# Optimization experiments

Measured on AMD Instinct MI355X. Metric: run time of the kernel, lower is better.

Reference implementation:

```python
import jax, jax.numpy as jnp
import numpy as np

M, I, J = 524288, 16, 16


def setup_inputs() -> dict:
    key = jax.random.key(0)
    k1, k2, k3, k4 = jax.random.split(key, 4)
    h = jax.random.normal(k1, (2, 1, 1, I, J), dtype=jnp.float32)
    gi = jax.random.normal(k2, (2, M, 1, I), dtype=jnp.float32)
    gj = jax.random.normal(k3, (2, 1, M, J), dtype=jnp.float32)
    theta = jax.random.uniform(k4, (2, M), dtype=jnp.float32) * (2.0 * np.pi)
    return {"h": h, "gi": gi, "gj": gj, "theta": theta}


def reference(h, gi, gj, theta):
    # Theta = diag(cos(theta[0])) + 1j * diag(sin(theta[1])) -- diagonal, so the
    # per-(i,j) bilinear form gj_j @ Theta @ gi_i is an O(M) contraction.
    tre = jnp.cos(theta[0])  # [M]
    tim = jnp.sin(theta[1])  # [M]
    a, b = gj[0, 0], gj[1, 0]            # [M, J] real/imag of gj
    e, f = gi[0, :, 0, :], gi[1, :, 0, :]  # [M, I] real/imag of gi
    # u = Theta_diag * gj (complex elementwise along M)
    u_re = a * tre[:, None] - b * tim[:, None]  # [M, J]
    u_im = a * tim[:, None] + b * tre[:, None]  # [M, J]
    # out[i,j] = sum_m gi[m,i] * theta[m] * gj[m,j] (complex)
    out_re = jnp.einsum('mi,mj->ij', e, u_re) - jnp.einsum('mi,mj->ij', f, u_im)
    out_im = jnp.einsum('mi,mj->ij', e, u_im) + jnp.einsum('mi,mj->ij', f, u_re)
    # htilde = h + reflected path, then squeeze the singleton dims -> [2, I, J]
    return h[:, 0, 0] + jnp.stack([out_re, out_im], axis=0)
```

## Files before the change

### kernel.cpp

```cpp
#include <hip/hip_runtime.h>


constexpr int MDIM    = 524288;
constexpr int THREADS = 256;
constexpr int BLOCKS  = 512;
constexpr int SLOTS   = BLOCKS * THREADS / 16;

__global__ void theta_init(const float* __restrict__ h, float* __restrict__ out) {
    int k = blockIdx.x * blockDim.x + threadIdx.x;
    if (k < 512) out[k] = h[k];
}

__device__ __forceinline__ void theta_step(
    const float4 e4, const float4 f4, const float4 a4, const float4 b4,
    const float c, const float s,
    float (&are)[4][4], float (&aim)[4][4])
{
    const float av[4] = {a4.x, a4.y, a4.z, a4.w};
    const float bv[4] = {b4.x, b4.y, b4.z, b4.w};
    const float ev[4] = {e4.x, e4.y, e4.z, e4.w};
    const float fv[4] = {f4.x, f4.y, f4.z, f4.w};
    float ure[4], uim[4];
#pragma unroll
    for (int j = 0; j < 4; ++j) {
        ure[j] = av[j] * c - bv[j] * s;
        uim[j] = av[j] * s + bv[j] * c;
    }
#pragma unroll
    for (int i = 0; i < 4; ++i) {
#pragma unroll
        for (int j = 0; j < 4; ++j) {
            are[i][j] += ev[i] * ure[j] - fv[i] * uim[j];
            aim[i][j] += ev[i] * uim[j] + fv[i] * ure[j];
        }
    }
}

__global__ __launch_bounds__(THREADS) void theta_main(
    const float* __restrict__ gi, const float* __restrict__ gj,
    const float* __restrict__ theta, float* __restrict__ out)
{
    const int t    = threadIdx.x;
    const int g    = blockIdx.x * THREADS + t;
    const int tile = t & 15;
    const int i0   = (tile >> 2) << 2;
    const int j0   = (tile & 3) << 2;
    const int slot = g >> 4;

    const float* e_base = gi + i0;
    const float* f_base = gi + MDIM * 16 + i0;
    const float* a_base = gj + j0;
    const float* b_base = gj + MDIM * 16 + j0;

    float are[4][4] = {{0.f}};
    float aim[4][4] = {{0.f}};

    for (int m = slot; m < MDIM; m += 2 * SLOTS) {
        const int m2 = m + SLOTS;
        const float4 e0 = *(const float4*)(e_base + m * 16);
        const float4 f0 = *(const float4*)(f_base + m * 16);
        const float4 a0 = *(const float4*)(a_base + m * 16);
        const float4 b0 = *(const float4*)(b_base + m * 16);
        const float t00 = theta[m];
        const float t10 = theta[MDIM + m];
        const float4 e1 = *(const float4*)(e_base + m2 * 16);
        const float4 f1 = *(const float4*)(f_base + m2 * 16);
        const float4 a1 = *(const float4*)(a_base + m2 * 16);
        const float4 b1 = *(const float4*)(b_base + m2 * 16);
        const float t01 = theta[m2];
        const float t11 = theta[MDIM + m2];

        const float c0 = __cosf(t00), s0 = __sinf(t10);
        theta_step(e0, f0, a0, b0, c0, s0, are, aim);
        const float c1 = __cosf(t01), s1 = __sinf(t11);
        theta_step(e1, f1, a1, b1, c1, s1, are, aim);
    }

#pragma unroll
    for (int i = 0; i < 4; ++i) {
#pragma unroll
        for (int j = 0; j < 4; ++j) {
            are[i][j] += __shfl_xor(are[i][j], 16);
            are[i][j] += __shfl_xor(are[i][j], 32);
            aim[i][j] += __shfl_xor(aim[i][j], 16);
            aim[i][j] += __shfl_xor(aim[i][j], 32);
        }
    }

    __shared__ float red[4][16][33];
    const int wave = t >> 6;
    const int lane = t & 63;
    if (lane < 16) {
#pragma unroll
        for (int i = 0; i < 4; ++i) {
#pragma unroll
            for (int j = 0; j < 4; ++j) {
                red[wave][lane][i * 4 + j]      = are[i][j];
                red[wave][lane][16 + i * 4 + j] = aim[i][j];
            }
        }
    }
    __syncthreads();

#pragma unroll
    for (int k = 0; k < 2; ++k) {
        const int idx = t * 2 + k;
        const int tl  = idx >> 5;
        const int v   = idx & 31;
        const float sum = red[0][tl][v] + red[1][tl][v] + red[2][tl][v] + red[3][tl][v];
        const int ii  = ((tl >> 2) << 2) + ((v & 15) >> 2);
        const int jj  = ((tl & 3) << 2) + (v & 3);
        const int off = ((v & 16) ? 256 : 0) + ii * 16 + jj;
        atomicAdd(out + off, sum);
    }
}

extern "C" void kernel_launch(void* const* d_in, const int* in_sizes, int n_in,
                              void* d_out, int out_size, void* d_ws, size_t ws_size,
                              hipStream_t stream) {
    const float* h     = (const float*)d_in[0];
    const float* gi    = (const float*)d_in[1];
    const float* gj    = (const float*)d_in[2];
    const float* theta = (const float*)d_in[3];
    float* out = (float*)d_out;

    theta_init<<<2, 256, 0, stream>>>(h, out);
    theta_main<<<BLOCKS, THREADS, 0, stream>>>(gi, gj, theta, out);
}
```

Measured before the change: 174.8 us.

## Quadruple grid, add occupancy hint, replace atomics with workspace partial reduction

Raises the grid from 512 to 2048 blocks with an 8-waves launch bound to increase memory-level parallelism on the bandwidth-bound contraction. When workspace is available, each block writes its 512 partial sums to a buffer and a separate reduce kernel adds them plus h, avoiding atomics and the init kernel. Risks register spilling from the occupancy bound and an extra launch with strided partial reads; falls back to the atomic path if workspace is too small.

After: 312.2 us. +78.6%, slower.

```diff
diff --git a/kernel.cpp b/kernel.cpp
--- a/kernel.cpp
+++ b/kernel.cpp
@@ -3,13 +3,8 @@
 
 constexpr int MDIM    = 524288;
 constexpr int THREADS = 256;
-constexpr int BLOCKS  = 512;
+constexpr int BLOCKS  = 2048;
 constexpr int SLOTS   = BLOCKS * THREADS / 16;
-
-__global__ void theta_init(const float* __restrict__ h, float* __restrict__ out) {
-    int k = blockIdx.x * blockDim.x + threadIdx.x;
-    if (k < 512) out[k] = h[k];
-}
 
 __device__ __forceinline__ void theta_step(
     const float4 e4, const float4 f4, const float4 a4, const float4 b4,
@@ -36,9 +31,10 @@
     }
 }
 
-__global__ __launch_bounds__(THREADS) void theta_main(
+template <bool USE_ATOMIC>
+__device__ __forceinline__ void theta_body(
     const float* __restrict__ gi, const float* __restrict__ gj,
-    const float* __restrict__ theta, float* __restrict__ out)
+    const float* __restrict__ theta, float* __restrict__ dst )
 {
     const int t    = threadIdx.x;
     const int g    = blockIdx.x * THREADS + t;
@@ -111,8 +107,43 @@
         const int ii  = ((tl >> 2) << 2) + ((v & 15) >> 2);
         const int jj  = ((tl & 3) << 2) + (v & 3);
         const int off = ((v & 16) ? 256 : 0) + ii * 16 + jj;
-        atomicAdd(out + off, sum);
+        if (USE_ATOMIC) atomicAdd(dst + off, sum);
+        else            dst[blockIdx.x * 512 + off] = sum;
     }
+}
+
+__global__ __launch_bounds__(THREADS, 8) void theta_main_ws(
+    const float* __restrict__ gi, const float* __restrict__ gj,
+    const float* __restrict__ theta, float* __restrict__ partial)
+{
+    theta_body<false>(gi, gj, theta, partial);
+}
+
+__global__ __launch_bounds__(THREADS, 8) void theta_main_atomic(
+    const float* __restrict__ gi, const float* __restrict__ gj,
+    const float* __restrict__ theta, float* __restrict__ out)
+{
+    theta_body<true>(gi, gj, theta, out);
+}
+
+__global__ __launch_bounds__(256) void theta_reduce(
+    const float* __restrict__ h, const float* __restrict__ partial,
+    float* __restrict__ out)
+{
+    const int w    = (blockIdx.x * 256 + threadIdx.x) >> 6;
+    const int lane = threadIdx.x & 63;
+    float s = 0.f;
+#pragma unroll 8
+    for (int j = 0; j < BLOCKS / 64; ++j)
+        s += partial[(j * 64 + lane) * 512 + w];
+#pragma unroll
+    for (int d = 1; d < 64; d <<= 1) s += __shfl_xor(s, d);
+    if (lane == 0) out[w] = h[w] + s;
+}
+
+__global__ void theta_init(const float* __restrict__ h, float* __restrict__ out) {
+    int k = blockIdx.x * blockDim.x + threadIdx.x;
+    if (k < 512) out[k] = h[k];
 }
 
 extern "C" void kernel_launch(void* const* d_in, const int* in_sizes, int n_in,
@@ -124,6 +155,13 @@
     const float* theta = (const float*)d_in[3];
     float* out = (float*)d_out;
 
-    theta_init<<<2, 256, 0, stream>>>(h, out);
-    theta_main<<<BLOCKS, THREADS, 0, stream>>>(gi, gj, theta, out);
+    const size_t need = (size_t)BLOCKS * 512 * sizeof(float);
+    if (ws_size >= need) {
+        float* partial = (float*)d_ws;
+        theta_main_ws<<<BLOCKS, THREADS, 0, stream>>>(gi, gj, theta, partial);
+        theta_reduce<<<128, 256, 0, stream>>>(h, partial, out);
+    } else {
+        theta_init<<<2, 256, 0, stream>>>(h, out);
+        theta_main_atomic<<<BLOCKS, THREADS, 0, stream>>>(gi, gj, theta, out);
+    }
 }
```
